# Performance work log

Measured on AMD Instinct MI355X. Metric: run time of the kernel, lower is better.

The kernel has to match this reference:

```python
import jax, jax.numpy as jnp
import numpy as np

B, N, C = 128, 36, 1024
K_NB = 16            # neighbors per node (top-k, includes loop)
KERNEL = 8           # number of Gaussian kernels
OUT = 1024           # out_dim; per-kernel out = OUT // KERNEL
PI = np.float32(np.pi)


def setup_inputs() -> dict:
    key = jax.random.key(0)
    ks = jax.random.split(key, 9)
    node_feats = jax.random.normal(ks[0], (B, N, C), dtype=jnp.float32)
    node_centre = jax.random.uniform(ks[1], (B, N, 2), dtype=jnp.float32)
    neighbor_idx = jax.random.randint(ks[2], (B * N, K_NB), 0, B * N, dtype=jnp.int32)
    graph_weights = jax.random.uniform(ks[3], (B * N * K_NB, 1), dtype=jnp.float32)
    # Gaussian kernel params (per reset_parameters)
    mean_rho = jax.random.uniform(ks[4], (1, KERNEL), dtype=jnp.float32)
    mean_theta = jax.random.uniform(ks[5], (1, KERNEL), minval=-PI, maxval=PI, dtype=jnp.float32)
    precision_rho = jax.random.uniform(ks[6], (1, KERNEL), minval=0.5, maxval=1.0, dtype=jnp.float32)
    precision_theta = jax.random.uniform(ks[7], (1, KERNEL), minval=0.5, maxval=1.0, dtype=jnp.float32)
    # per-kernel Linear(node_dim, out_dim//kernel, bias=False), stacked: [K, d_out_k, C]
    conv_w = jax.random.normal(ks[8], (KERNEL, OUT // KERNEL, C), dtype=jnp.float32) * (1.0 / np.sqrt(C))
    return {
        "node_feats": node_feats,
        "node_centre": node_centre,
        "neighbor_idx": neighbor_idx,
        "graph_weights": graph_weights,
        "mean_rho": mean_rho,
        "mean_theta": mean_theta,
        "precision_rho": precision_rho,
        "precision_theta": precision_theta,
        "conv_w": conv_w,
    }


def _forward(node_feats, node_centre, graph_weights,
             mean_rho, mean_theta, precision_rho, precision_theta,
             conv_w, neighbor_idx):
    b, n, c = node_feats.shape
    bn = b * n
    # pseudo polar coordinates per edge: centre_i - centre_j
    centre = node_centre.reshape(bn, 2)                       # [BN, 2]
    diff = centre[:, None, :] - centre[neighbor_idx]          # [BN, K_nb, 2]
    coord_x = diff[..., 0].reshape(-1)                        # [E]
    coord_y = diff[..., 1].reshape(-1)
    rho = jnp.sqrt(coord_x ** 2 + coord_y ** 2)
    theta = jnp.arctan2(coord_x, coord_y)
    # Gaussian mixture membership weights over KERNEL kernels
    w_rho = jnp.exp(-0.5 * (rho[:, None] - mean_rho) ** 2 / (1e-14 + precision_rho ** 2))
    first_angle = jnp.abs(theta[:, None] - mean_theta)
    second_angle = jnp.abs(2.0 * PI - first_angle)
    w_theta = jnp.exp(-0.5 * jnp.minimum(first_angle, second_angle) ** 2 / (1e-14 + precision_theta ** 2))
    weights = w_rho * w_theta                                  # [E, KERNEL]
    weights = jnp.where(jnp.isnan(weights), 0.0, weights)
    weights = weights / jnp.sum(weights, axis=1, keepdims=True)
    # combine with graph edge weights
    edge_w = graph_weights * weights                           # [E, KERNEL]
    edge_w = edge_w.reshape(bn, K_NB, KERNEL).transpose(0, 2, 1)  # [BN, K, K_nb]
    # gather neighbor features and weighted aggregate (bmm)
    nbr = node_feats.reshape(bn, c)[neighbor_idx]              # [BN, K_nb, C]
    agg = jnp.einsum('ekn,enc->ekc', edge_w, nbr)              # [BN, KERNEL, C]
    agg = agg.reshape(b, n, KERNEL, c)
    # per-kernel linear then concat over kernel dim
    out = jnp.einsum('bnkc,kdc->bnkd', agg, conv_w)            # [B, N, KERNEL, OUT//KERNEL]
    out = out.reshape(b, n, -1)                                # [B, N, OUT]
    return jax.nn.relu(out)


def reference(node_feats, node_centre, neighbor_idx, graph_weights,
              mean_rho, mean_theta, precision_rho, precision_theta, conv_w):
    return _forward(node_feats, node_centre, graph_weights,
                    mean_rho, mean_theta, precision_rho, precision_theta,
                    conv_w, neighbor_idx)
```

## Files before the change

### kernel.cpp

```cpp
#include <hip/hip_runtime.h>
#include <hip/hip_bf16.h>
#include <stdint.h>

#define B_DIM   128
#define N_DIM   36
#define C_DIM   1024
#define KNB     16
#define NKER    8
#define OUTD    1024
#define BN_NODES (B_DIM * N_DIM)
#define E_EDGES  (BN_NODES * KNB)
#define PI_F 3.14159265358979323846f

#define TM 64
#define TN 128
#define BK 64
#define KIT (C_DIM / BK)
#define CLP 136
#define A_OFF(p) ((p) * TM * BK)
#define B_OFF(p) (2 * TM * BK + (p) * TN * BK)

typedef __attribute__((ext_vector_type(8))) short bf16x8;
typedef __attribute__((ext_vector_type(4))) float floatx4;

struct alignas(8) U16x4 { unsigned short x, y, z, w; };

__device__ __forceinline__ unsigned short f2bf(float f) {
  union { float f; uint32_t u; } v; v.f = f;
  uint32_t u = v.u;
  return (unsigned short)((u + 0x7fffu + ((u >> 16) & 1u)) >> 16);
}
__device__ __forceinline__ float bf2f_lo(uint32_t pair) {
  union { uint32_t u; float f; } v; v.u = pair << 16;
  return v.f;
}
__device__ __forceinline__ float bf2f_hi(uint32_t pair) {
  union { uint32_t u; float f; } v; v.u = pair & 0xffff0000u;
  return v.f;
}

__device__ __forceinline__ void gload16(const void* g, void* l) {
  __builtin_amdgcn_global_load_lds((__attribute__((address_space(1))) void*)(g),
                                   (__attribute__((address_space(3))) void*)(l),
                                   16, 0, 0);
}

__global__ __launch_bounds__(256)
void cast_kernel(const float* __restrict__ feats,
                 const float* __restrict__ cw,
                 unsigned short* __restrict__ fb,
                 unsigned short* __restrict__ wb)
{
  const int NF4 = (BN_NODES * C_DIM) / 4;
  const int NW4 = (C_DIM * OUTD) / 4;
  int tid = blockIdx.x * 256 + threadIdx.x;
  if (tid < NF4) {
    float4 v = ((const float4*)feats)[tid];
    U16x4 o = { f2bf(v.x), f2bf(v.y), f2bf(v.z), f2bf(v.w) };
    ((U16x4*)fb)[tid] = o;
  } else {
    int t = tid - NF4;
    if (t < NW4) {
      float4 v = ((const float4*)cw)[t];
      U16x4 o = { f2bf(v.x), f2bf(v.y), f2bf(v.z), f2bf(v.w) };
      ((U16x4*)wb)[t] = o;
    }
  }
}

__global__ __launch_bounds__(256)
void gemm_bt(const unsigned short* __restrict__ A,
             const unsigned short* __restrict__ Bt,
             unsigned short* __restrict__ D)
{
  __shared__ unsigned short smem[2 * TM * BK + 2 * TN * BK];

  const int tid  = threadIdx.x;
  const int lane = tid & 63;
  const int wave = tid >> 6;
  const int wm   = wave >> 1;
  const int wn   = wave & 1;
  const int row0 = blockIdx.x * TM;
  const int col0 = blockIdx.y * TN;

  const int q  = lane >> 4;
  const int lr = lane & 15;

  floatx4 acc[2][4] = {};

  int offA[2], offB[4];
#pragma unroll
  for (int i = 0; i < 2; ++i) {
    int c = tid + 256 * i, row = c >> 3, qc = c & 7;
    offA[i] = (row0 + row) * C_DIM + (qc ^ (row & 7)) * 8;
  }
#pragma unroll
  for (int i = 0; i < 4; ++i) {
    int c = tid + 256 * i, row = c >> 3, qc = c & 7;
    offB[i] = (col0 + row) * C_DIM + (qc ^ (row & 7)) * 8;
  }

#define DMA(T, P) do {                                                       \
    _Pragma("unroll") for (int i = 0; i < 2; ++i)                            \
      gload16(A + offA[i] + (T) * BK,                                        \
              &smem[A_OFF(P) + (tid + 256 * i) * 8]);                        \
    _Pragma("unroll") for (int i = 0; i < 4; ++i)                            \
      gload16(Bt + offB[i] + (T) * BK,                                       \
              &smem[B_OFF(P) + (tid + 256 * i) * 8]);                        \
  } while (0)

  DMA(0, 0);

  for (int t = 0; t < KIT; ++t) {
    const int p = t & 1;
    __syncthreads();
    if (t + 1 < KIT) DMA(t + 1, 1 - p);

    const int aBase = A_OFF(p);
    const int bBase = B_OFF(p);
#pragma unroll
    for (int kc = 0; kc < 2; ++kc) {
      const int sc = ((kc * 4 + q) ^ (lr & 7)) * 8;
      bf16x8 af[2], bfr[4];
#pragma unroll
      for (int i = 0; i < 2; ++i)
        af[i]  = *(const bf16x8*)&smem[aBase + (wm * 32 + i * 16 + lr) * BK + sc];
#pragma unroll
      for (int j = 0; j < 4; ++j)
        bfr[j] = *(const bf16x8*)&smem[bBase + (wn * 64 + j * 16 + lr) * BK + sc];
#pragma unroll
      for (int i = 0; i < 2; ++i)
#pragma unroll
        for (int j = 0; j < 4; ++j)
          acc[i][j] = __builtin_amdgcn_mfma_f32_16x16x32_bf16(
              af[i], bfr[j], acc[i][j], 0, 0, 0);
    }
  }
#undef DMA

  __syncthreads();
#pragma unroll
  for (int i = 0; i < 2; ++i)
#pragma unroll
    for (int j = 0; j < 4; ++j)
#pragma unroll
      for (int r = 0; r < 4; ++r)
        smem[(wm * 32 + i * 16 + q * 4 + r) * CLP + wn * 64 + j * 16 + lr] =
            f2bf(acc[i][j][r]);
  __syncthreads();
#pragma unroll
  for (int i = 0; i < 4; ++i) {
    int c = tid + 256 * i;
    int row = c >> 4, qc = c & 15;
    *(uint4*)&D[(size_t)(row0 + row) * OUTD + col0 + qc * 8] =
        *(const uint4*)&smem[row * CLP + qc * 8];
  }
}

__global__ __launch_bounds__(256)
void agg_fused(const unsigned short* __restrict__ proj,
               const float* __restrict__ centre,
               const int*   __restrict__ nbr,
               const float* __restrict__ gw,
               const float* __restrict__ mrho,
               const float* __restrict__ mth,
               const float* __restrict__ prho,
               const float* __restrict__ pth,
               float* __restrict__ out)
{
  __shared__ int   idx[2][KNB];
  __shared__ float nxy[2][KNB][2];
  __shared__ float cxy[2][2];
  __shared__ float wk[2][KNB][NKER];
  __shared__ float scl[2][KNB];
  __shared__ float ew[2][NKER][KNB];

  const int n0   = blockIdx.x * 2;
  const int t    = threadIdx.x;
  const int half = t >> 7;
  const int u    = t & 127;

  if (t < 32) {
    int h = t >> 4, j = t & 15;
    int m = nbr[(n0 + h) * KNB + j];
    idx[h][j] = m;
    nxy[h][j][0] = centre[2 * m];
    nxy[h][j][1] = centre[2 * m + 1];
  } else if (t < 34) {
    int h = t - 32;
    cxy[h][0] = centre[2 * (n0 + h)];
    cxy[h][1] = centre[2 * (n0 + h) + 1];
  }
  __syncthreads();

  {
    int j = u >> 3, k = u & 7;
    float cx = cxy[half][0] - nxy[half][j][0];
    float cy = cxy[half][1] - nxy[half][j][1];
    float rho   = sqrtf(cx * cx + cy * cy);
    float theta = atan2f(cx, cy);
    float dr = rho - mrho[k];
    float pr = prho[k];
    float w_r = expf(-0.5f * dr * dr / (1e-14f + pr * pr));
    float fa = fabsf(theta - mth[k]);
    float sa = fabsf(2.0f * PI_F - fa);
    float mm = fminf(fa, sa);
    float pt = pth[k];
    float w_t = expf(-0.5f * mm * mm / (1e-14f + pt * pt));
    float ww = w_r * w_t;
    wk[half][j][k] = (ww != ww) ? 0.f : ww;
  }
  __syncthreads();

  if (u < KNB) {
    float s = 0.f;
#pragma unroll
    for (int k = 0; k < NKER; ++k) s += wk[half][u][k];
    scl[half][u] = gw[(n0 + half) * KNB + u] / s;
  }
  __syncthreads();

  {
    int j = u >> 3, k = u & 7;
    ew[half][k][j] = wk[half][j][k] * scl[half][j];
  }
  __syncthreads();

  const int n = n0 + half;
  const int k = u >> 4;
  float a[8] = {0.f, 0.f, 0.f, 0.f, 0.f, 0.f, 0.f, 0.f};
#pragma unroll
  for (int j = 0; j < KNB; ++j) {
    float wv = ew[half][k][j];
    uint4 v = *(const uint4*)&proj[(size_t)idx[half][j] * OUTD + u * 8];
    a[0] += wv * bf2f_lo(v.x);  a[1] += wv * bf2f_hi(v.x);
    a[2] += wv * bf2f_lo(v.y);  a[3] += wv * bf2f_hi(v.y);
    a[4] += wv * bf2f_lo(v.z);  a[5] += wv * bf2f_hi(v.z);
    a[6] += wv * bf2f_lo(v.w);  a[7] += wv * bf2f_hi(v.w);
  }
  float4 r0, r1;
  r0.x = fmaxf(a[0], 0.f); r0.y = fmaxf(a[1], 0.f);
  r0.z = fmaxf(a[2], 0.f); r0.w = fmaxf(a[3], 0.f);
  r1.x = fmaxf(a[4], 0.f); r1.y = fmaxf(a[5], 0.f);
  r1.z = fmaxf(a[6], 0.f); r1.w = fmaxf(a[7], 0.f);
  float* o = out + (size_t)n * OUTD + u * 8;
  *(float4*)(o)     = r0;
  *(float4*)(o + 4) = r1;
}

extern "C" void kernel_launch(void* const* d_in, const int* in_sizes, int n_in,
                              void* d_out, int out_size, void* d_ws, size_t ws_size,
                              hipStream_t stream)
{
  const float* feats  = (const float*)d_in[0];
  const float* centre = (const float*)d_in[1];
  const int*   nbr    = (const int*)  d_in[2];
  const float* gw     = (const float*)d_in[3];
  const float* mrho   = (const float*)d_in[4];
  const float* mth    = (const float*)d_in[5];
  const float* prho   = (const float*)d_in[6];
  const float* pth    = (const float*)d_in[7];
  const float* cw     = (const float*)d_in[8];
  float* out = (float*)d_out;

  char* ws = (char*)d_ws;
  unsigned short* fb   = (unsigned short*)(ws);
  unsigned short* wb   = (unsigned short*)(ws + 9437184);
  unsigned short* proj = (unsigned short*)(ws + 11534336);

  cast_kernel<<<dim3(((BN_NODES * C_DIM) / 4 + (C_DIM * OUTD) / 4) / 256),
                dim3(256), 0, stream>>>(feats, cw, fb, wb);
  gemm_bt<<<dim3(BN_NODES / TM, OUTD / TN), dim3(256), 0, stream>>>(fb, wb, proj);
  agg_fused<<<dim3(BN_NODES / 2), dim3(256), 0, stream>>>(
      proj, centre, nbr, gw, mrho, mth, prho, pth, out);
}
```

Baseline: 121.7 us.

## Fuse fp32-to-bf16 feature cast into GEMM A-tile loading

Removes the separate cast pass over node features. The GEMM now loads fp32 A tiles into registers, converts them to bf16 and writes them to LDS after the MFMA loop, which overlaps the next tile's load with compute. This cuts a full write and re-read of the bf16 feature buffer. The cost is that each A tile is re-read in fp32 by all column blocks (8x, at twice the bytes), and the A path loses the async direct-to-LDS loads and needs extra registers.

```diff
diff --git a/kernel.cpp b/kernel.cpp
--- a/kernel.cpp
+++ b/kernel.cpp
@@ -23,7 +23,8 @@
 typedef __attribute__((ext_vector_type(8))) short bf16x8;
 typedef __attribute__((ext_vector_type(4))) float floatx4;
 
-struct alignas(8) U16x4 { unsigned short x, y, z, w; };
+struct alignas(8)  U16x4 { unsigned short x, y, z, w; };
+struct alignas(16) U16x8 { U16x4 lo, hi; };
 
 __device__ __forceinline__ unsigned short f2bf(float f) {
   union { float f; uint32_t u; } v; v.f = f;
@@ -46,30 +47,17 @@
 }
 
 __global__ __launch_bounds__(256)
-void cast_kernel(const float* __restrict__ feats,
-                 const float* __restrict__ cw,
-                 unsigned short* __restrict__ fb,
-                 unsigned short* __restrict__ wb)
-{
-  const int NF4 = (BN_NODES * C_DIM) / 4;
-  const int NW4 = (C_DIM * OUTD) / 4;
+void cast_wb(const float* __restrict__ cw,
+             unsigned short* __restrict__ wb)
+{
   int tid = blockIdx.x * 256 + threadIdx.x;
-  if (tid < NF4) {
-    float4 v = ((const float4*)feats)[tid];
-    U16x4 o = { f2bf(v.x), f2bf(v.y), f2bf(v.z), f2bf(v.w) };
-    ((U16x4*)fb)[tid] = o;
-  } else {
-    int t = tid - NF4;
-    if (t < NW4) {
-      float4 v = ((const float4*)cw)[t];
-      U16x4 o = { f2bf(v.x), f2bf(v.y), f2bf(v.z), f2bf(v.w) };
-      ((U16x4*)wb)[t] = o;
-    }
-  }
+  float4 v = ((const float4*)cw)[tid];
+  U16x4 o = { f2bf(v.x), f2bf(v.y), f2bf(v.z), f2bf(v.w) };
+  ((U16x4*)wb)[tid] = o;
 }
 
 __global__ __launch_bounds__(256)
-void gemm_bt(const unsigned short* __restrict__ A,
+void gemm_bt(const float* __restrict__ Af,
              const unsigned short* __restrict__ Bt,
              unsigned short* __restrict__ D)
 {
@@ -88,33 +76,54 @@
 
   floatx4 acc[2][4] = {};
 
-  int offA[2], offB[4];
+  int offAf[2], ldsA[2];
 #pragma unroll
   for (int i = 0; i < 2; ++i) {
     int c = tid + 256 * i, row = c >> 3, qc = c & 7;
-    offA[i] = (row0 + row) * C_DIM + (qc ^ (row & 7)) * 8;
-  }
+    offAf[i] = (row0 + row) * C_DIM + (qc ^ (row & 7)) * 8;
+    ldsA[i]  = c * 8;
+  }
+  int offB[4];
 #pragma unroll
   for (int i = 0; i < 4; ++i) {
     int c = tid + 256 * i, row = c >> 3, qc = c & 7;
     offB[i] = (col0 + row) * C_DIM + (qc ^ (row & 7)) * 8;
   }
 
-#define DMA(T, P) do {                                                       \
-    _Pragma("unroll") for (int i = 0; i < 2; ++i)                            \
-      gload16(A + offA[i] + (T) * BK,                                        \
-              &smem[A_OFF(P) + (tid + 256 * i) * 8]);                        \
+  float4 aReg[2][2];
+
+#define LDA(T) do {                                                          \
+    _Pragma("unroll") for (int i = 0; i < 2; ++i) {                          \
+      aReg[i][0] = *(const float4*)(Af + offAf[i] + (T) * BK);               \
+      aReg[i][1] = *(const float4*)(Af + offAf[i] + (T) * BK + 4);           \
+    }                                                                        \
+  } while (0)
+
+#define STA(P) do {                                                          \
+    _Pragma("unroll") for (int i = 0; i < 2; ++i) {                          \
+      U16x8 o;                                                               \
+      o.lo.x = f2bf(aReg[i][0].x); o.lo.y = f2bf(aReg[i][0].y);              \
+      o.lo.z = f2bf(aReg[i][0].z); o.lo.w = f2bf(aReg[i][0].w);              \
+      o.hi.x = f2bf(aReg[i][1].x); o.hi.y = f2bf(aReg[i][1].y);              \
+      o.hi.z = f2bf(aReg[i][1].z); o.hi.w = f2bf(aReg[i][1].w);              \
+      *(U16x8*)&smem[A_OFF(P) + ldsA[i]] = o;                                \
+    }                                                                        \
+  } while (0)
+
+#define DMAB(T, P) do {                                                      \
     _Pragma("unroll") for (int i = 0; i < 4; ++i)                            \
       gload16(Bt + offB[i] + (T) * BK,                                       \
               &smem[B_OFF(P) + (tid + 256 * i) * 8]);                        \
   } while (0)
 
-  DMA(0, 0);
+  LDA(0);
+  DMAB(0, 0);
+  STA(0);
 
   for (int t = 0; t < KIT; ++t) {
     const int p = t & 1;
     __syncthreads();
-    if (t + 1 < KIT) DMA(t + 1, 1 - p);
+    if (t + 1 < KIT) { LDA(t + 1); DMAB(t + 1, 1 - p); }
 
     const int aBase = A_OFF(p);
     const int bBase = B_OFF(p);
@@ -135,8 +144,11 @@
           acc[i][j] = __builtin_amdgcn_mfma_f32_16x16x32_bf16(
               af[i], bfr[j], acc[i][j], 0, 0, 0);
     }
-  }
-#undef DMA
+    if (t + 1 < KIT) STA(1 - p);
+  }
+#undef LDA
+#undef STA
+#undef DMAB
 
   __syncthreads();
 #pragma unroll
@@ -264,13 +276,11 @@
   float* out = (float*)d_out;
 
   char* ws = (char*)d_ws;
-  unsigned short* fb   = (unsigned short*)(ws);
-  unsigned short* wb   = (unsigned short*)(ws + 9437184);
-  unsigned short* proj = (unsigned short*)(ws + 11534336);
-
-  cast_kernel<<<dim3(((BN_NODES * C_DIM) / 4 + (C_DIM * OUTD) / 4) / 256),
-                dim3(256), 0, stream>>>(feats, cw, fb, wb);
-  gemm_bt<<<dim3(BN_NODES / TM, OUTD / TN), dim3(256), 0, stream>>>(fb, wb, proj);
+  unsigned short* wb   = (unsigned short*)(ws);
+  unsigned short* proj = (unsigned short*)(ws + 2097152);
+
+  cast_wb<<<dim3((C_DIM * OUTD) / 4 / 256), dim3(256), 0, stream>>>(cw, wb);
+  gemm_bt<<<dim3(BN_NODES / TM, OUTD / TN), dim3(256), 0, stream>>>(feats, wb, proj);
   agg_fused<<<dim3(BN_NODES / 2), dim3(256), 0, stream>>>(
       proj, centre, nbr, gw, mrho, mth, prho, pth, out);
 }
```

Measured after the change: 123.8 us. Within noise of the previous version (+1.7%).
